# Kernel tuning notes

Measured on AMD Instinct MI355X. Metric: run time of the kernel, lower is better.

## Reference

```python
import jax, jax.numpy as jnp
import numpy as np

EMBED_DIM = 512
SE_HIDDEN = max(1, int(EMBED_DIM * 0.25))  # 128
LN_EPS = 1e-5


def setup_inputs() -> dict:
    key = jax.random.key(0)
    ks = jax.random.split(key, 16)
    B, H, W, D = 8, 32, 32, EMBED_DIM
    s = 0.02
    return {
        "q": jax.random.normal(ks[0], (B, H, W, D), jnp.float32),
        "k": jax.random.normal(ks[1], (B, H, W, D), jnp.float32),
        "v": jax.random.normal(ks[2], (B, H, W, D), jnp.float32),
        # Linear weights stored as [in, out] (equivalent to torch W.T)
        "Wq": jax.random.normal(ks[3], (D, D), jnp.float32) * s,
        "Wk": jax.random.normal(ks[4], (D, D), jnp.float32) * s,
        "Wv": jax.random.normal(ks[5], (D, D), jnp.float32) * s,
        "Wo": jax.random.normal(ks[6], (D, D), jnp.float32) * s,
        # Conv2d kernel in HWIO layout for NHWC conv
        "conv_w": jax.random.normal(ks[7], (3, 3, D, D), jnp.float32) * s,
        "conv_b": jnp.zeros((D,), jnp.float32),
        "se_w1": jax.random.normal(ks[8], (D, SE_HIDDEN), jnp.float32) * s,
        "se_b1": jnp.zeros((SE_HIDDEN,), jnp.float32),
        "se_w2": jax.random.normal(ks[9], (SE_HIDDEN, D), jnp.float32) * s,
        "se_b2": jnp.zeros((D,), jnp.float32),
        "ln_g": jnp.ones((D,), jnp.float32),
        "ln_b": jnp.zeros((D,), jnp.float32),
    }


def _layernorm(x, g, b):
    mu = jnp.mean(x, axis=-1, keepdims=True)
    var = jnp.mean(jnp.square(x - mu), axis=-1, keepdims=True)
    return (x - mu) * jax.lax.rsqrt(var + LN_EPS) * g + b


def reference(q, k, v, Wq, Wk, Wv, Wo, conv_w, conv_b,
              se_w1, se_b1, se_w2, se_b2, ln_g, ln_b):
    B, H, W, D = q.shape
    scaler = jnp.sqrt(jnp.asarray(D, q.dtype))
    qp = q @ Wq  # [B,H,W,D]
    kp = k @ Wk
    vp = v @ Wv
    N = H * W
    qf = qp.reshape(B, N, D)
    kf = kp.reshape(B, N, D)
    vf = vp.reshape(B, N, D)
    scores = jnp.einsum('bnd,bmd->bnm', qf, kf) / scaler
    probs = jax.nn.softmax(scores, axis=-1)  # dropout p=0 -> identity
    out = jnp.einsum('bnm,bmd->bnd', probs, vf).reshape(B, H, W, D)
    out = out @ Wo
    # 3x3 same conv in NHWC
    out = jax.lax.conv_general_dilated(
        out, conv_w, window_strides=(1, 1), padding='SAME',
        dimension_numbers=('NHWC', 'HWIO', 'NHWC')) + conv_b
    # squeeze-excite: global average pool over spatial dims
    se = jnp.mean(out, axis=(1, 2))  # [B,D]
    se = jax.nn.silu(se @ se_w1 + se_b1)
    se = jax.nn.sigmoid(se @ se_w2 + se_b2)  # [B,D]
    out = out * se[:, None, None, :]
    x = qp + out  # residual uses q AFTER q_proj (q reassigned in torch code)
    return _layernorm(x, ln_g, ln_b)
```

## Files before the change

kernel.cpp:

```cpp
#include <hip/hip_runtime.h>
#include <hip/hip_bf16.h>

using bf16 = __hip_bfloat16;
typedef __attribute__((ext_vector_type(8))) short short8;
typedef __attribute__((ext_vector_type(4))) short short4v;
typedef __attribute__((ext_vector_type(4))) float f32x4;

static const size_t OFF_QP   = 0;
static const size_t OFF_KP   = (size_t)8  << 20;
static const size_t OFF_VPT  = (size_t)16 << 20;
static const size_t OFF_SC   = (size_t)24 << 20;
static const size_t OFF_WT   = (size_t)56 << 20;
static const size_t OFF_CWT  = (size_t)58 << 20;
static const size_t OFF_POOL = (size_t)63 << 20;
static const size_t OFF_SE   = ((size_t)63 << 20) + 16384;

__global__ __launch_bounds__(256) void prep_k(const float* __restrict__ Wq,
                                              const float* __restrict__ Wk,
                                              const float* __restrict__ Wv,
                                              const float* __restrict__ Wo,
                                              const float* __restrict__ convw,
                                              bf16* __restrict__ wT,
                                              bf16* __restrict__ cwT,
                                              float* __restrict__ pooled) {
    long idx = (long)blockIdx.x * 256 + threadIdx.x;
    if (idx < 4l * 262144) {
        int m = (int)(idx >> 18);
        int o = (int)(idx & 262143);
        int n = o >> 9, k = o & 511;
        const float* W = (m == 0) ? Wq : (m == 1) ? Wk : (m == 2) ? Wv : Wo;
        wT[idx] = __float2bfloat16(W[k * 512 + n]);
    } else if (idx < 4l * 262144 + 512l * 4608) {
        long o = idx - 4l * 262144;
        int co = (int)(o / 4608), t = (int)(o % 4608);
        cwT[o] = __float2bfloat16(convw[(long)t * 512 + co]);
    } else if (idx < 4l * 262144 + 512l * 4608 + 4096) {
        pooled[idx - (4l * 262144 + 512l * 4608)] = 0.f;
    }
}

template <int OP>
__global__ __launch_bounds__(256, 2) void gemm_k(
    const void* __restrict__ Ap0, const void* __restrict__ Ap1, const void* __restrict__ Ap2,
    int lda, long sA,
    const bf16* __restrict__ BT, int ldb, long sB,
    void* __restrict__ Cp, int ldc, long sC,
    int K, const float* __restrict__ bias, float* __restrict__ pooled) {
    __shared__ bf16 As[2][128 * 64];
    __shared__ bf16 Bs[2][64 * 64];
    const int tid = threadIdx.x;
    const int l = tid & 63, w = tid >> 6;
    const int wm = w >> 1, wn = w & 1;

    const int gx = gridDim.x, gy = gridDim.y;
    const int nwg = gx * gy * gridDim.z;
    const int bid = blockIdx.x + gx * (blockIdx.y + gy * blockIdx.z);
    const int swz = (bid & 7) * (nwg >> 3) + (bid >> 3);
    const int bx = swz % gx;
    const int rem = swz / gx;
    const int by = rem % gy;
    const int zb = rem / gy;

    const int m0 = by * 128, n0 = bx * 64;
    const float isc = 0.04419417382415922f;

    const bf16* Ab = nullptr;
    const float* Af = nullptr;
    if (OP == 1) {
        Af = (const float*)(zb == 0 ? Ap0 : zb == 1 ? Ap1 : Ap2);
    } else {
        Ab = (const bf16*)Ap0 + (long)zb * sA;
    }
    const bf16* Bb = BT + (OP == 1 ? (long)zb * 262144 : (long)zb * sB);

    const int fr = l & 15;
    f32x4 acc[4][2] = {};

    int pixoff[4], hh_[4], wp_[4];
    if (OP == 3) {
#pragma unroll
        for (int i = 0; i < 4; ++i) {
            int s = tid + i * 256;
            int row = s >> 3, c = s & 7;
            int p = m0 + row;
            int bb = p >> 10;
            hh_[i] = (p >> 5) & 31;
            wp_[i] = p & 31;
            pixoff[i] = ((bb * 32 + hh_[i]) * 32 + wp_[i]) * 512 + c * 8;
        }
    }

    struct SR {
        short8 ar[4];
        float4 af0[4], af1[4];
        short8 br[2];
    };
    SR S0, S1, S2, S3;

    auto stage_load = [&](int t, SR& S) {
        int k0 = t * 64;
        int dy = 0, dx = 0, doff = 0;
        if (OP == 3) {
            int tap = k0 >> 9;
            dy = tap / 3 - 1;
            dx = tap % 3 - 1;
            doff = (dy * 32 + dx) * 512 + (k0 & 511);
        }
#pragma unroll
        for (int i = 0; i < 4; ++i) {
            int s = tid + i * 256;
            int row = s >> 3, c = s & 7;
            if (OP == 1) {
                const float* src = Af + (long)(m0 + row) * lda + k0 + c * 8;
                S.af0[i] = *(const float4*)src;
                S.af1[i] = *(const float4*)(src + 4);
            } else if (OP == 3) {
                int h2 = hh_[i] + dy, w2 = wp_[i] + dx;
                if (((unsigned)h2 < 32u) & ((unsigned)w2 < 32u)) {
                    S.ar[i] = *(const short8*)(Ab + pixoff[i] + doff);
                } else {
                    short8 zz = {0, 0, 0, 0, 0, 0, 0, 0};
                    S.ar[i] = zz;
                }
            } else {
                S.ar[i] = *(const short8*)(Ab + (long)(m0 + row) * lda + k0 + c * 8);
            }
        }
#pragma unroll
        for (int i = 0; i < 2; ++i) {
            int s = tid + i * 256;
            int row = s >> 3, c = s & 7;
            S.br[i] = *(const short8*)(Bb + (long)(n0 + row) * ldb + k0 + c * 8);
        }
    };

    auto stage_write = [&](int b, SR& S) {
#pragma unroll
        for (int i = 0; i < 4; ++i) {
            int s = tid + i * 256;
            int row = s >> 3, c = s & 7;
            int cx = c ^ (row & 7);
            if (OP == 1) {
                union { short8 s8; bf16 h[8]; } u;
                u.h[0] = __float2bfloat16(S.af0[i].x); u.h[1] = __float2bfloat16(S.af0[i].y);
                u.h[2] = __float2bfloat16(S.af0[i].z); u.h[3] = __float2bfloat16(S.af0[i].w);
                u.h[4] = __float2bfloat16(S.af1[i].x); u.h[5] = __float2bfloat16(S.af1[i].y);
                u.h[6] = __float2bfloat16(S.af1[i].z); u.h[7] = __float2bfloat16(S.af1[i].w);
                *(short8*)(&As[b][row * 64 + cx * 8]) = u.s8;
            } else {
                *(short8*)(&As[b][row * 64 + cx * 8]) = S.ar[i];
            }
        }
#pragma unroll
        for (int i = 0; i < 2; ++i) {
            int s = tid + i * 256;
            int row = s >> 3, c = s & 7;
            int cx = c ^ (row & 7);
            *(short8*)(&Bs[b][row * 64 + cx * 8]) = S.br[i];
        }
    };

    auto compute = [&](int b) {
#pragma unroll
        for (int h = 0; h < 2; ++h) {
            int cx = ((l >> 4) + 4 * h) ^ (fr & 7);
            short8 afr[4], bfv[2];
#pragma unroll
            for (int m = 0; m < 4; ++m) {
                int r = wm * 64 + m * 16 + fr;
                afr[m] = *(const short8*)(&As[b][r * 64 + cx * 8]);
            }
#pragma unroll
            for (int n = 0; n < 2; ++n) {
                int r = wn * 32 + n * 16 + fr;
                bfv[n] = *(const short8*)(&Bs[b][r * 64 + cx * 8]);
            }
#pragma unroll
            for (int m = 0; m < 4; ++m)
#pragma unroll
                for (int n = 0; n < 2; ++n)
                    acc[m][n] = __builtin_amdgcn_mfma_f32_16x16x32_bf16(afr[m], bfv[n], acc[m][n], 0, 0, 0);
        }
    };

    const int nt = K >> 6;
    stage_load(0, S0);
    stage_load(1, S1);
    stage_load(2, S2);
    stage_load(3, S3);
    stage_write(0, S0);
    for (int t = 0; t < nt; t += 4) {
        __syncthreads();
        if (t + 4 < nt) stage_load(t + 4, S0);
        compute(0);
        stage_write(1, S1);
        __syncthreads();
        if (t + 5 < nt) stage_load(t + 5, S1);
        compute(1);
        stage_write(0, S2);
        __syncthreads();
        if (t + 6 < nt) stage_load(t + 6, S2);
        compute(0);
        stage_write(1, S3);
        __syncthreads();
        if (t + 7 < nt) stage_load(t + 7, S3);
        compute(1);
        if (t + 4 < nt) stage_write(0, S0);
    }

    const int cr = (l >> 4) * 4, cc = l & 15;
    float csum[2] = {0.f, 0.f};
#pragma unroll
    for (int m = 0; m < 4; ++m) {
#pragma unroll
        for (int n = 0; n < 2; ++n) {
#pragma unroll
            for (int j = 0; j < 4; ++j) {
                int r = m0 + wm * 64 + m * 16 + cr + j;
                int c = n0 + wn * 32 + n * 16 + cc;
                float vv = acc[m][n][j];
                if (OP == 3) {
                    vv += bias[c];
                    csum[n] += vv;
                    ((bf16*)Cp)[(long)r * ldc + c] = __float2bfloat16(vv);
                } else if (OP == 0 || OP == 2) {
                    ((bf16*)Cp)[(long)zb * sC + (long)r * ldc + c] = __float2bfloat16(vv);
                } else {
                    if (zb == 2) {
                        ((bf16*)Cp)[(size_t)(OFF_VPT / 2) + ((long)(r >> 10) * 512 + c) * 1024 + (r & 1023)] =
                            __float2bfloat16(vv);
                    } else {
                        float sv = (zb == 1) ? vv * isc : vv;
                        ((bf16*)Cp)[(long)zb * 4194304 + (long)r * 512 + c] = __float2bfloat16(sv);
                    }
                }
            }
        }
    }
    if (OP == 3) {
        int bb = m0 >> 10;
#pragma unroll
        for (int n = 0; n < 2; ++n) {
            int c = n0 + wn * 32 + n * 16 + cc;
            atomicAdd(&pooled[bb * 512 + c], csum[n] * (1.0f / 1024.0f));
        }
    }
}

__global__ __launch_bounds__(256) void softmax_k(bf16* __restrict__ scores) {
    __shared__ float red[256];
    long row = blockIdx.x;
    bf16* base = scores + row * 1024;
    int t = threadIdx.x;
    union { short4v s4; bf16 h[4]; } u;
    u.s4 = *(const short4v*)(base + t * 4);
    float v[4];
#pragma unroll
    for (int i = 0; i < 4; ++i) v[i] = __bfloat162float(u.h[i]);
    float mx = fmaxf(fmaxf(v[0], v[1]), fmaxf(v[2], v[3]));
    red[t] = mx;
    __syncthreads();
    for (int s = 128; s > 0; s >>= 1) {
        if (t < s) red[t] = fmaxf(red[t], red[t + s]);
        __syncthreads();
    }
    mx = red[0];
    __syncthreads();
    float e[4], sum = 0.f;
#pragma unroll
    for (int i = 0; i < 4; ++i) {
        e[i] = __expf(v[i] - mx);
        sum += e[i];
    }
    red[t] = sum;
    __syncthreads();
    for (int s = 128; s > 0; s >>= 1) {
        if (t < s) red[t] += red[t + s];
        __syncthreads();
    }
    float inv = 1.0f / red[0];
#pragma unroll
    for (int i = 0; i < 4; ++i) u.h[i] = __float2bfloat16(e[i] * inv);
    *(short4v*)(base + t * 4) = u.s4;
}

__global__ __launch_bounds__(512) void se_mlp_k(const float* __restrict__ pooled,
                                                const float* __restrict__ w1,
                                                const float* __restrict__ b1,
                                                const float* __restrict__ w2,
                                                const float* __restrict__ b2,
                                                float* __restrict__ se) {
    __shared__ float pl[512];
    __shared__ float part[4][128];
    __shared__ float hid[128];
    const int b = blockIdx.x, t = threadIdx.x;
    pl[t] = pooled[b * 512 + t];
    __syncthreads();
    const int j = t & 127, r = t >> 7;
    float acc = 0.f;
#pragma unroll 8
    for (int s = 0; s < 128; ++s) {
        int i = r * 128 + s;
        acc += pl[i] * w1[i * 128 + j];
    }
    part[r][j] = acc;
    __syncthreads();
    if (t < 128) {
        float a = part[0][t] + part[1][t] + part[2][t] + part[3][t] + b1[t];
        hid[t] = a / (1.f + __expf(-a));
    }
    __syncthreads();
    float acc2 = b2[t];
#pragma unroll 8
    for (int jj = 0; jj < 128; ++jj)
        acc2 += hid[jj] * w2[jj * 512 + t];
    se[b * 512 + t] = 1.f / (1.f + __expf(-acc2));
}

__global__ __launch_bounds__(256) void final_k(const bf16* __restrict__ conv_out,
                                               const float* __restrict__ se,
                                               const bf16* __restrict__ qp,
                                               const float* __restrict__ g,
                                               const float* __restrict__ bta,
                                               float* __restrict__ out) {
    __shared__ float red[256];
    long p = blockIdx.x;
    int b = (int)(p >> 10);
    int t = threadIdx.x;
    float x[2];
#pragma unroll
    for (int i = 0; i < 2; ++i) {
        int c = t + i * 256;
        x[i] = __bfloat162float(qp[p * 512 + c]) +
               __bfloat162float(conv_out[p * 512 + c]) * se[b * 512 + c];
    }
    red[t] = x[0] + x[1];
    __syncthreads();
    for (int s = 128; s > 0; s >>= 1) {
        if (t < s) red[t] += red[t + s];
        __syncthreads();
    }
    float mu = red[0] * (1.0f / 512.0f);
    __syncthreads();
    float d0 = x[0] - mu, d1 = x[1] - mu;
    red[t] = d0 * d0 + d1 * d1;
    __syncthreads();
    for (int s = 128; s > 0; s >>= 1) {
        if (t < s) red[t] += red[t + s];
        __syncthreads();
    }
    float inv = rsqrtf(red[0] * (1.0f / 512.0f) + 1e-5f);
#pragma unroll
    for (int i = 0; i < 2; ++i) {
        int c = t + i * 256;
        out[p * 512 + c] = (x[i] - mu) * inv * g[c] + bta[c];
    }
}

extern "C" void kernel_launch(void* const* d_in, const int* in_sizes, int n_in,
                              void* d_out, int out_size, void* d_ws, size_t ws_size,
                              hipStream_t stream) {
    const float* q      = (const float*)d_in[0];
    const float* k      = (const float*)d_in[1];
    const float* v      = (const float*)d_in[2];
    const float* Wq     = (const float*)d_in[3];
    const float* Wk     = (const float*)d_in[4];
    const float* Wv     = (const float*)d_in[5];
    const float* Wo     = (const float*)d_in[6];
    const float* convw  = (const float*)d_in[7];
    const float* convb  = (const float*)d_in[8];
    const float* se_w1  = (const float*)d_in[9];
    const float* se_b1  = (const float*)d_in[10];
    const float* se_w2  = (const float*)d_in[11];
    const float* se_b2  = (const float*)d_in[12];
    const float* ln_g   = (const float*)d_in[13];
    const float* ln_b   = (const float*)d_in[14];

    char* ws = (char*)d_ws;
    bf16*  qp     = (bf16*)(ws + OFF_QP);
    bf16*  kp     = (bf16*)(ws + OFF_KP);
    bf16*  attn   = (bf16*)(ws + OFF_KP);
    bf16*  vpT    = (bf16*)(ws + OFF_VPT);
    bf16*  out2   = (bf16*)(ws + OFF_VPT);
    bf16*  scores = (bf16*)(ws + OFF_SC);
    bf16*  convo  = (bf16*)(ws + OFF_SC);
    bf16*  wT     = (bf16*)(ws + OFF_WT);
    bf16*  cwT    = (bf16*)(ws + OFF_CWT);
    float* pooled = (float*)(ws + OFF_POOL);
    float* se     = (float*)(ws + OFF_SE);

    prep_k<<<13328, 256, 0, stream>>>(Wq, Wk, Wv, Wo, convw, wT, cwT, pooled);

    gemm_k<1><<<dim3(8, 64, 3), 256, 0, stream>>>(q, k, v, 512, 0, wT, 512, 0,
                                                  ws, 512, 0, 512, nullptr, nullptr);
    gemm_k<2><<<dim3(16, 8, 8), 256, 0, stream>>>(qp, nullptr, nullptr, 512, 1024l * 512,
                                                  kp, 512, 1024l * 512,
                                                  scores, 1024, 1024l * 1024, 512, nullptr, nullptr);
    softmax_k<<<8192, 256, 0, stream>>>(scores);
    gemm_k<0><<<dim3(8, 8, 8), 256, 0, stream>>>(scores, nullptr, nullptr, 1024, 1024l * 1024,
                                                 vpT, 1024, 512l * 1024,
                                                 attn, 512, 1024l * 512, 1024, nullptr, nullptr);
    gemm_k<0><<<dim3(8, 64, 1), 256, 0, stream>>>(attn, nullptr, nullptr, 512, 0,
                                                  wT + 3 * 262144, 512, 0,
                                                  out2, 512, 0, 512, nullptr, nullptr);
    gemm_k<3><<<dim3(8, 64, 1), 256, 0, stream>>>(out2, nullptr, nullptr, 0, 0,
                                                  cwT, 4608, 0,
                                                  convo, 512, 0, 4608, convb, pooled);
    se_mlp_k<<<8, 512, 0, stream>>>(pooled, se_w1, se_b1, se_w2, se_b2, se);
    final_k<<<8192, 256, 0, stream>>>(convo, se, qp, ln_g, ln_b, (float*)d_out);
}
```

Before: 203.8 us.

## Split conv implicit-GEMM over K with larger 128x128 tiles and fp32 partials

Replaces the templated conv path with a dedicated conv kernel that uses 128x128 output tiles with K-step 32, and splits the 4608-long reduction into two halves across grid z. Each half writes fp32 partial sums to separate buffers. The final LayerNorm kernel sums the two partials. Pooling is done by atomics from both halves. The larger tiles give more reuse per block and the split keeps the grid at 512 blocks. The cost is a bigger fp32 partial buffer (about 32 MB written and then read back) in place of a bf16 output.

```diff
diff --git a/kernel.cpp b/kernel.cpp
--- a/kernel.cpp
+++ b/kernel.cpp
@@ -45,7 +45,7 @@
     int lda, long sA,
     const bf16* __restrict__ BT, int ldb, long sB,
     void* __restrict__ Cp, int ldc, long sC,
-    int K, const float* __restrict__ bias, float* __restrict__ pooled) {
+    int K) {
     __shared__ bf16 As[2][128 * 64];
     __shared__ bf16 Bs[2][64 * 64];
     const int tid = threadIdx.x;
@@ -76,20 +76,6 @@
     const int fr = l & 15;
     f32x4 acc[4][2] = {};
 
-    int pixoff[4], hh_[4], wp_[4];
-    if (OP == 3) {
-#pragma unroll
-        for (int i = 0; i < 4; ++i) {
-            int s = tid + i * 256;
-            int row = s >> 3, c = s & 7;
-            int p = m0 + row;
-            int bb = p >> 10;
-            hh_[i] = (p >> 5) & 31;
-            wp_[i] = p & 31;
-            pixoff[i] = ((bb * 32 + hh_[i]) * 32 + wp_[i]) * 512 + c * 8;
-        }
-    }
-
     struct SR {
         short8 ar[4];
         float4 af0[4], af1[4];
@@ -99,13 +85,6 @@
 
     auto stage_load = [&](int t, SR& S) {
         int k0 = t * 64;
-        int dy = 0, dx = 0, doff = 0;
-        if (OP == 3) {
-            int tap = k0 >> 9;
-            dy = tap / 3 - 1;
-            dx = tap % 3 - 1;
-            doff = (dy * 32 + dx) * 512 + (k0 & 511);
-        }
 #pragma unroll
         for (int i = 0; i < 4; ++i) {
             int s = tid + i * 256;
@@ -114,14 +93,6 @@
                 const float* src = Af + (long)(m0 + row) * lda + k0 + c * 8;
                 S.af0[i] = *(const float4*)src;
                 S.af1[i] = *(const float4*)(src + 4);
-            } else if (OP == 3) {
-                int h2 = hh_[i] + dy, w2 = wp_[i] + dx;
-                if (((unsigned)h2 < 32u) & ((unsigned)w2 < 32u)) {
-                    S.ar[i] = *(const short8*)(Ab + pixoff[i] + doff);
-                } else {
-                    short8 zz = {0, 0, 0, 0, 0, 0, 0, 0};
-                    S.ar[i] = zz;
-                }
             } else {
                 S.ar[i] = *(const short8*)(Ab + (long)(m0 + row) * lda + k0 + c * 8);
             }
@@ -209,7 +180,6 @@
     }
 
     const int cr = (l >> 4) * 4, cc = l & 15;
-    float csum[2] = {0.f, 0.f};
 #pragma unroll
     for (int m = 0; m < 4; ++m) {
 #pragma unroll
@@ -219,11 +189,7 @@
                 int r = m0 + wm * 64 + m * 16 + cr + j;
                 int c = n0 + wn * 32 + n * 16 + cc;
                 float vv = acc[m][n][j];
-                if (OP == 3) {
-                    vv += bias[c];
-                    csum[n] += vv;
-                    ((bf16*)Cp)[(long)r * ldc + c] = __float2bfloat16(vv);
-                } else if (OP == 0 || OP == 2) {
+                if (OP == 0 || OP == 2) {
                     ((bf16*)Cp)[(long)zb * sC + (long)r * ldc + c] = __float2bfloat16(vv);
                 } else {
                     if (zb == 2) {
@@ -237,13 +203,156 @@
             }
         }
     }
-    if (OP == 3) {
-        int bb = m0 >> 10;
-#pragma unroll
-        for (int n = 0; n < 2; ++n) {
-            int c = n0 + wn * 32 + n * 16 + cc;
-            atomicAdd(&pooled[bb * 512 + c], csum[n] * (1.0f / 1024.0f));
-        }
+}
+
+__global__ __launch_bounds__(256, 2) void conv_k(
+    const bf16* __restrict__ A,
+    const bf16* __restrict__ BT,
+    float* __restrict__ P,
+    const float* __restrict__ bias,
+    float* __restrict__ pooled) {
+    __shared__ bf16 As[2][128 * 32];
+    __shared__ bf16 Bs[2][128 * 32];
+    const int tid = threadIdx.x;
+    const int l = tid & 63, w = tid >> 6;
+    const int wm = w >> 1, wn = w & 1;
+
+    const int gx = 4, gy = 64, nwg = 512;
+    const int bid = blockIdx.x + gx * (blockIdx.y + gy * blockIdx.z);
+    const int swz = (bid & 7) * (nwg >> 3) + (bid >> 3);
+    const int bx = swz % gx;
+    const int rem = swz / gx;
+    const int by = rem % gy;
+    const int zb = rem / gy;
+
+    const int m0 = by * 128, n0 = bx * 128;
+    const int kbase = zb * 2304;
+
+    const int fr = l & 15;
+    const int ck = (l >> 4) ^ ((fr >> 1) & 3);
+    f32x4 acc[4][4] = {};
+
+    int pixoff[2], hh_[2], wp_[2];
+#pragma unroll
+    for (int i = 0; i < 2; ++i) {
+        int s = tid + i * 256;
+        int row = s >> 2, c = s & 3;
+        int p = m0 + row;
+        int bb = p >> 10;
+        hh_[i] = (p >> 5) & 31;
+        wp_[i] = p & 31;
+        pixoff[i] = ((bb * 32 + hh_[i]) * 32 + wp_[i]) * 512 + c * 8;
+    }
+
+    struct SR { short8 ar[2]; short8 br[2]; };
+    SR S0, S1, S2, S3;
+
+    auto stage_load = [&](int t, SR& S) {
+        int k0 = kbase + t * 32;
+        int tap = k0 >> 9;
+        int dy = tap / 3 - 1, dx = tap % 3 - 1;
+        int doff = (dy * 32 + dx) * 512 + (k0 & 511);
+#pragma unroll
+        for (int i = 0; i < 2; ++i) {
+            int h2 = hh_[i] + dy, w2 = wp_[i] + dx;
+            if (((unsigned)h2 < 32u) & ((unsigned)w2 < 32u)) {
+                S.ar[i] = *(const short8*)(A + pixoff[i] + doff);
+            } else {
+                short8 zz = {0, 0, 0, 0, 0, 0, 0, 0};
+                S.ar[i] = zz;
+            }
+        }
+#pragma unroll
+        for (int i = 0; i < 2; ++i) {
+            int s = tid + i * 256;
+            int row = s >> 2, c = s & 3;
+            S.br[i] = *(const short8*)(BT + (long)(n0 + row) * 4608 + k0 + c * 8);
+        }
+    };
+
+    auto stage_write = [&](int b, SR& S) {
+#pragma unroll
+        for (int i = 0; i < 2; ++i) {
+            int s = tid + i * 256;
+            int row = s >> 2, c = s & 3;
+            int c2 = c ^ ((row >> 1) & 3);
+            *(short8*)(&As[b][row * 32 + c2 * 8]) = S.ar[i];
+        }
+#pragma unroll
+        for (int i = 0; i < 2; ++i) {
+            int s = tid + i * 256;
+            int row = s >> 2, c = s & 3;
+            int c2 = c ^ ((row >> 1) & 3);
+            *(short8*)(&Bs[b][row * 32 + c2 * 8]) = S.br[i];
+        }
+    };
+
+    auto compute = [&](int b) {
+        short8 af[4], bf[4];
+#pragma unroll
+        for (int m = 0; m < 4; ++m) {
+            int r = wm * 64 + m * 16 + fr;
+            af[m] = *(const short8*)(&As[b][r * 32 + ck * 8]);
+        }
+#pragma unroll
+        for (int n = 0; n < 4; ++n) {
+            int r = wn * 64 + n * 16 + fr;
+            bf[n] = *(const short8*)(&Bs[b][r * 32 + ck * 8]);
+        }
+#pragma unroll
+        for (int m = 0; m < 4; ++m)
+#pragma unroll
+            for (int n = 0; n < 4; ++n)
+                acc[m][n] = __builtin_amdgcn_mfma_f32_16x16x32_bf16(af[m], bf[n], acc[m][n], 0, 0, 0);
+    };
+
+    const int nt = 72;
+    stage_load(0, S0);
+    stage_load(1, S1);
+    stage_load(2, S2);
+    stage_load(3, S3);
+    stage_write(0, S0);
+    for (int t = 0; t < nt; t += 4) {
+        __syncthreads();
+        if (t + 4 < nt) stage_load(t + 4, S0);
+        compute(0);
+        stage_write(1, S1);
+        __syncthreads();
+        if (t + 5 < nt) stage_load(t + 5, S1);
+        compute(1);
+        stage_write(0, S2);
+        __syncthreads();
+        if (t + 6 < nt) stage_load(t + 6, S2);
+        compute(0);
+        stage_write(1, S3);
+        __syncthreads();
+        if (t + 7 < nt) stage_load(t + 7, S3);
+        compute(1);
+        if (t + 4 < nt) stage_write(0, S0);
+    }
+
+    const int cr = (l >> 4) * 4, cc = l & 15;
+    float csum[4] = {0.f, 0.f, 0.f, 0.f};
+#pragma unroll
+    for (int m = 0; m < 4; ++m) {
+#pragma unroll
+        for (int n = 0; n < 4; ++n) {
+#pragma unroll
+            for (int j = 0; j < 4; ++j) {
+                int r = m0 + wm * 64 + m * 16 + cr + j;
+                int c = n0 + wn * 64 + n * 16 + cc;
+                float vv = acc[m][n][j];
+                if (zb == 0) vv += bias[c];
+                csum[n] += vv;
+                P[(long)zb * 4194304 + (long)r * 512 + c] = vv;
+            }
+        }
+    }
+    int bb = m0 >> 10;
+#pragma unroll
+    for (int n = 0; n < 4; ++n) {
+        int c = n0 + wn * 64 + n * 16 + cc;
+        atomicAdd(&pooled[bb * 512 + c], csum[n] * (1.0f / 1024.0f));
     }
 }
 
@@ -317,7 +426,7 @@
     se[b * 512 + t] = 1.f / (1.f + __expf(-acc2));
 }
 
-__global__ __launch_bounds__(256) void final_k(const bf16* __restrict__ conv_out,
+__global__ __launch_bounds__(256) void final_k(const float* __restrict__ P,
                                                const float* __restrict__ se,
                                                const bf16* __restrict__ qp,
                                                const float* __restrict__ g,
@@ -331,8 +440,8 @@
 #pragma unroll
     for (int i = 0; i < 2; ++i) {
         int c = t + i * 256;
-        x[i] = __bfloat162float(qp[p * 512 + c]) +
-               __bfloat162float(conv_out[p * 512 + c]) * se[b * 512 + c];
+        float cv = P[p * 512 + c] + P[4194304 + p * 512 + c];
+        x[i] = __bfloat162float(qp[p * 512 + c]) + cv * se[b * 512 + c];
     }
     red[t] = x[0] + x[1];
     __syncthreads();
@@ -383,7 +492,7 @@
     bf16*  vpT    = (bf16*)(ws + OFF_VPT);
     bf16*  out2   = (bf16*)(ws + OFF_VPT);
     bf16*  scores = (bf16*)(ws + OFF_SC);
-    bf16*  convo  = (bf16*)(ws + OFF_SC);
+    float* convP  = (float*)(ws + OFF_SC);
     bf16*  wT     = (bf16*)(ws + OFF_WT);
     bf16*  cwT    = (bf16*)(ws + OFF_CWT);
     float* pooled = (float*)(ws + OFF_POOL);
@@ -392,20 +501,18 @@
     prep_k<<<13328, 256, 0, stream>>>(Wq, Wk, Wv, Wo, convw, wT, cwT, pooled);
 
     gemm_k<1><<<dim3(8, 64, 3), 256, 0, stream>>>(q, k, v, 512, 0, wT, 512, 0,
-                                                  ws, 512, 0, 512, nullptr, nullptr);
+                                                  ws, 512, 0, 512);
     gemm_k<2><<<dim3(16, 8, 8), 256, 0, stream>>>(qp, nullptr, nullptr, 512, 1024l * 512,
                                                   kp, 512, 1024l * 512,
-                                                  scores, 1024, 1024l * 1024, 512, nullptr, nullptr);
+                                                  scores, 1024, 1024l * 1024, 512);
     softmax_k<<<8192, 256, 0, stream>>>(scores);
     gemm_k<0><<<dim3(8, 8, 8), 256, 0, stream>>>(scores, nullptr, nullptr, 1024, 1024l * 1024,
                                                  vpT, 1024, 512l * 1024,
-                                                 attn, 512, 1024l * 512, 1024, nullptr, nullptr);
+                                                 attn, 512, 1024l * 512, 1024);
     gemm_k<0><<<dim3(8, 64, 1), 256, 0, stream>>>(attn, nullptr, nullptr, 512, 0,
                                                   wT + 3 * 262144, 512, 0,
-                                                  out2, 512, 0, 512, nullptr, nullptr);
-    gemm_k<3><<<dim3(8, 64, 1), 256, 0, stream>>>(out2, nullptr, nullptr, 0, 0,
-                                                  cwT, 4608, 0,
-                                                  convo, 512, 0, 4608, convb, pooled);
+                                                  out2, 512, 0, 512);
+    conv_k<<<dim3(4, 64, 2), 256, 0, stream>>>(out2, cwT, convP, convb, pooled);
     se_mlp_k<<<8, 512, 0, stream>>>(pooled, se_w1, se_b1, se_w2, se_b2, se);
-    final_k<<<8192, 256, 0, stream>>>(convo, se, qp, ln_g, ln_b, (float*)d_out);
-}
+    final_k<<<8192, 256, 0, stream>>>(convP, se, qp, ln_g, ln_b, (float*)d_out);
+}
```

Result: slower. 214.9 us (+5.4%).

## Fuse softmax into the PV GEMM and defer row normalization to the Wo GEMM

Applied to the files above, without the earlier changes.

Removes the standalone softmax kernel. The PV GEMM now exponentiates the raw bf16 scores while loading its A tiles, accumulates per-row exp sums, and writes reciprocal row sums to a workspace buffer. The following Wo projection GEMM scales each attention row by that reciprocal while loading, so the normalization moves out of a separate pass. This saves one full read and write of the score matrix and a kernel launch. In exchange the exp is recomputed redundantly by every column block, and dropping the max subtraction risks overflow if scores are large.

```diff
diff --git a/kernel.cpp b/kernel.cpp
--- a/kernel.cpp
+++ b/kernel.cpp
@@ -14,6 +14,7 @@
 static const size_t OFF_CWT  = (size_t)58 << 20;
 static const size_t OFF_POOL = (size_t)63 << 20;
 static const size_t OFF_SE   = ((size_t)63 << 20) + 16384;
+static const size_t OFF_RS   = ((size_t)63 << 20) + 32768;
 
 __global__ __launch_bounds__(256) void prep_k(const float* __restrict__ Wq,
                                               const float* __restrict__ Wk,
@@ -39,13 +40,20 @@
     }
 }
 
+__device__ __forceinline__ float bf2f(unsigned short h) {
+    union { unsigned int u; float f; } c;
+    c.u = (unsigned int)h << 16;
+    return c.f;
+}
+
 template <int OP>
 __global__ __launch_bounds__(256, 2) void gemm_k(
     const void* __restrict__ Ap0, const void* __restrict__ Ap1, const void* __restrict__ Ap2,
     int lda, long sA,
     const bf16* __restrict__ BT, int ldb, long sB,
     void* __restrict__ Cp, int ldc, long sC,
-    int K, const float* __restrict__ bias, float* __restrict__ pooled) {
+    int K, const float* __restrict__ bias, float* __restrict__ pooled,
+    float* __restrict__ rs) {
     __shared__ bf16 As[2][128 * 64];
     __shared__ bf16 Bs[2][64 * 64];
     const int tid = threadIdx.x;
@@ -75,6 +83,7 @@
 
     const int fr = l & 15;
     f32x4 acc[4][2] = {};
+    float esum[4] = {0.f, 0.f, 0.f, 0.f};
 
     int pixoff[4], hh_[4], wp_[4];
     if (OP == 3) {
@@ -122,6 +131,30 @@
                     short8 zz = {0, 0, 0, 0, 0, 0, 0, 0};
                     S.ar[i] = zz;
                 }
+            } else if (OP == 4) {
+                union { short8 s8; unsigned short h[8]; } u, o;
+                u.s8 = *(const short8*)(Ab + (long)(m0 + row) * lda + k0 + c * 8);
+                float es = 0.f;
+#pragma unroll
+                for (int j = 0; j < 8; ++j) {
+                    float e = __expf(bf2f(u.h[j]));
+                    es += e;
+                    union { float f; unsigned int ui; } cf;
+                    cf.f = e;
+                    o.h[j] = (unsigned short)(cf.ui >> 16);
+                }
+                esum[i] += es;
+                S.ar[i] = o.s8;
+            } else if (OP == 5) {
+                float rinv = rs[m0 + row];
+                union { short8 s8; unsigned short h[8]; } u, o;
+                u.s8 = *(const short8*)(Ab + (long)(m0 + row) * lda + k0 + c * 8);
+#pragma unroll
+                for (int j = 0; j < 8; ++j) {
+                    bf16 b = __float2bfloat16(bf2f(u.h[j]) * rinv);
+                    o.h[j] = *(unsigned short*)&b;
+                }
+                S.ar[i] = o.s8;
             } else {
                 S.ar[i] = *(const short8*)(Ab + (long)(m0 + row) * lda + k0 + c * 8);
             }
@@ -208,6 +241,23 @@
         if (t + 4 < nt) stage_write(0, S0);
     }
 
+    if (OP == 4) {
+        __syncthreads();
+        float* fl = (float*)&As[0][0];
+#pragma unroll
+        for (int i = 0; i < 4; ++i) {
+            int s = tid + i * 256;
+            fl[(s >> 3) * 8 + (s & 7)] = esum[i];
+        }
+        __syncthreads();
+        if (bx == 0 && tid < 128) {
+            float s8 = 0.f;
+#pragma unroll
+            for (int j = 0; j < 8; ++j) s8 += fl[tid * 8 + j];
+            rs[zb * 1024 + m0 + tid] = 1.0f / s8;
+        }
+    }
+
     const int cr = (l >> 4) * 4, cc = l & 15;
     float csum[2] = {0.f, 0.f};
 #pragma unroll
@@ -223,7 +273,7 @@
                     vv += bias[c];
                     csum[n] += vv;
                     ((bf16*)Cp)[(long)r * ldc + c] = __float2bfloat16(vv);
-                } else if (OP == 0 || OP == 2) {
+                } else if (OP != 1) {
                     ((bf16*)Cp)[(long)zb * sC + (long)r * ldc + c] = __float2bfloat16(vv);
                 } else {
                     if (zb == 2) {
@@ -245,43 +295,6 @@
             atomicAdd(&pooled[bb * 512 + c], csum[n] * (1.0f / 1024.0f));
         }
     }
-}
-
-__global__ __launch_bounds__(256) void softmax_k(bf16* __restrict__ scores) {
-    __shared__ float red[256];
-    long row = blockIdx.x;
-    bf16* base = scores + row * 1024;
-    int t = threadIdx.x;
-    union { short4v s4; bf16 h[4]; } u;
-    u.s4 = *(const short4v*)(base + t * 4);
-    float v[4];
-#pragma unroll
-    for (int i = 0; i < 4; ++i) v[i] = __bfloat162float(u.h[i]);
-    float mx = fmaxf(fmaxf(v[0], v[1]), fmaxf(v[2], v[3]));
-    red[t] = mx;
-    __syncthreads();
-    for (int s = 128; s > 0; s >>= 1) {
-        if (t < s) red[t] = fmaxf(red[t], red[t + s]);
-        __syncthreads();
-    }
-    mx = red[0];
-    __syncthreads();
-    float e[4], sum = 0.f;
-#pragma unroll
-    for (int i = 0; i < 4; ++i) {
-        e[i] = __expf(v[i] - mx);
-        sum += e[i];
-    }
-    red[t] = sum;
-    __syncthreads();
-    for (int s = 128; s > 0; s >>= 1) {
-        if (t < s) red[t] += red[t + s];
-        __syncthreads();
-    }
-    float inv = 1.0f / red[0];
-#pragma unroll
-    for (int i = 0; i < 4; ++i) u.h[i] = __float2bfloat16(e[i] * inv);
-    *(short4v*)(base + t * 4) = u.s4;
 }
 
 __global__ __launch_bounds__(512) void se_mlp_k(const float* __restrict__ pooled,
@@ -388,24 +401,24 @@
     bf16*  cwT    = (bf16*)(ws + OFF_CWT);
     float* pooled = (float*)(ws + OFF_POOL);
     float* se     = (float*)(ws + OFF_SE);
+    float* rsinv  = (float*)(ws + OFF_RS);
 
     prep_k<<<13328, 256, 0, stream>>>(Wq, Wk, Wv, Wo, convw, wT, cwT, pooled);
 
     gemm_k<1><<<dim3(8, 64, 3), 256, 0, stream>>>(q, k, v, 512, 0, wT, 512, 0,
-                                                  ws, 512, 0, 512, nullptr, nullptr);
+                                                  ws, 512, 0, 512, nullptr, nullptr, nullptr);
     gemm_k<2><<<dim3(16, 8, 8), 256, 0, stream>>>(qp, nullptr, nullptr, 512, 1024l * 512,
                                                   kp, 512, 1024l * 512,
-                                                  scores, 1024, 1024l * 1024, 512, nullptr, nullptr);
-    softmax_k<<<8192, 256, 0, stream>>>(scores);
-    gemm_k<0><<<dim3(8, 8, 8), 256, 0, stream>>>(scores, nullptr, nullptr, 1024, 1024l * 1024,
+                                                  scores, 1024, 1024l * 1024, 512, nullptr, nullptr, nullptr);
+    gemm_k<4><<<dim3(8, 8, 8), 256, 0, stream>>>(scores, nullptr, nullptr, 1024, 1024l * 1024,
                                                  vpT, 1024, 512l * 1024,
-                                                 attn, 512, 1024l * 512, 1024, nullptr, nullptr);
-    gemm_k<0><<<dim3(8, 64, 1), 256, 0, stream>>>(attn, nullptr, nullptr, 512, 0,
+                                                 attn, 512, 1024l * 512, 1024, nullptr, nullptr, rsinv);
+    gemm_k<5><<<dim3(8, 64, 1), 256, 0, stream>>>(attn, nullptr, nullptr, 512, 0,
                                                   wT + 3 * 262144, 512, 0,
-                                                  out2, 512, 0, 512, nullptr, nullptr);
+                                                  out2, 512, 0, 512, nullptr, nullptr, rsinv);
     gemm_k<3><<<dim3(8, 64, 1), 256, 0, stream>>>(out2, nullptr, nullptr, 0, 0,
                                                   cwT, 4608, 0,
-                                                  convo, 512, 0, 4608, convb, pooled);
+                                                  convo, 512, 0, 4608, convb, pooled, nullptr);
     se_mlp_k<<<8, 512, 0, stream>>>(pooled, se_w1, se_b1, se_w2, se_b2, se);
     final_k<<<8192, 256, 0, stream>>>(convo, se, qp, ln_g, ln_b, (float*)d_out);
 }
```

Result: no change. 200.2 us (-1.8%).
